# Optimization experiments

Hardware: AMD Instinct MI355X
Metric: run time of the kernel (lower is better)

## Reference

```python
import jax, jax.numpy as jnp
import numpy as np

K = 8               # config.k
X_MIN = -1.0        # x_min
X_MAX = 1.0         # x_max
GLOBAL_COEFF = 1.0  # config.global_coeff
EPS = 1e-8          # torch cosine_similarity eps
BZ, P, D = 8192, 1024, 1024  # batch, num_pool, data_dim


def setup_inputs() -> dict:
    key = jax.random.key(0)
    k1, k2, k3, k4, k5 = jax.random.split(key, 5)
    return {
        "ppg": jax.random.normal(k1, (BZ, 1, D), dtype=jnp.float32),
        "keys_pool": jax.random.normal(k2, (P, D), dtype=jnp.float32),
        "prompt_pool": jax.random.normal(k3, (P, D), dtype=jnp.float32),
        "cnn_w": jax.random.normal(k4, (1, 1, 3), dtype=jnp.float32) * 0.5,
        "cnn_b": jax.random.normal(k5, (1,), dtype=jnp.float32) * 0.1,
    }


def _prompt_cnn(prompt, w, b):
    # PromptCNN: Conv1d(1,1,k=3,pad=1) + ReLU on [P, D]
    x = prompt[:, None, :]  # [P, 1, D]
    y = jax.lax.conv_general_dilated(
        x, w, window_strides=(1,), padding=((1, 1),),
        dimension_numbers=("NCH", "OIH", "NCH"))
    y = jax.nn.relu(y + b[None, :, None])
    return y[:, 0, :]  # [P, D]


def _global_normalizer(prompt, x_min, x_max):
    pmax = jnp.max(prompt, axis=-1, keepdims=True)
    pmin = jnp.min(prompt, axis=-1, keepdims=True)
    scale = (x_max - x_min) / (pmax - pmin)
    return scale * (prompt - pmin) + x_min


def reference(ppg, keys_pool, prompt_pool, cnn_w, cnn_b):
    # prompt pool through CNN
    pcnn = _prompt_cnn(prompt_pool, cnn_w, cnn_b)  # [P, D]

    # cosine similarity: ppg [bz,1,D] vs keys [P,D] -> [bz,P]
    pn = ppg[:, 0, :] / jnp.maximum(
        jnp.linalg.norm(ppg[:, 0, :], axis=-1, keepdims=True), EPS)
    kn = keys_pool / jnp.maximum(
        jnp.linalg.norm(keys_pool, axis=-1, keepdims=True), EPS)
    cos = jnp.einsum("bd,pd->bp", pn, kn)  # [bz, P]
    score_ = 1.0 - cos

    # top-k smallest distances (largest=False) -> ascending order
    neg_vals, idx = jax.lax.top_k(-score_, K)  # [bz, K]
    score = -neg_vals

    # entropy of softmax over raw scores
    logp = jax.nn.log_softmax(score_, axis=-1)
    entropy = -(jnp.exp(logp) * logp).sum(axis=-1).mean()

    # gather selected prompts, average over k, add singleton channel dim
    prompt = pcnn[idx].mean(axis=1)[:, None, :]  # [bz, 1, D]

    # min-max global normalization (glonorm=True)
    prompt = _global_normalizer(prompt, X_MIN, X_MAX)

    # additive combine (mul=False)
    prompted = ppg + GLOBAL_COEFF * prompt  # [bz, 1, D]

    return prompted, score.mean(), entropy
```

## Files before the change

kernel.cpp:

```cpp
#include <hip/hip_runtime.h>
#include <hip/hip_bf16.h>

#define BZ 8192
#define PP 1024
#define DD 1024
#define KSEL 8

typedef unsigned short u16;
typedef __attribute__((ext_vector_type(8))) short bf16x8;
typedef __attribute__((ext_vector_type(4))) float f32x4;

#define WS_INVK 0
#define WS_INVP 1024
#define WS_SCORE 9216
#define WS_ENT 17408
#define WS_BF16_BYTE 368640ull

__device__ __forceinline__ u16 f2bf(float x) {
  __hip_bfloat16 h = __float2bfloat16(x);
  return *(u16*)&h;
}
__device__ __forceinline__ float bf2f(u16 u) {
  __hip_bfloat16 h; *(u16*)&h = u;
  return __bfloat162float(h);
}
__device__ __forceinline__ void gll16(const void* g, void* l) {
  __builtin_amdgcn_global_load_lds((__attribute__((address_space(1))) void*)g,
                                   (__attribute__((address_space(3))) void*)l, 16, 0, 0);
}

__global__ __launch_bounds__(256) void convert_kernel(const float* __restrict__ ppg,
                                                      const float* __restrict__ keys,
                                                      float* __restrict__ ws) {
  u16* Ahi = (u16*)((char*)ws + WS_BF16_BYTE);
  u16* Alo = Ahi + 8388608;
  u16* Bhi = Alo + 8388608;
  u16* Blo = Bhi + 1048576;

  int blk = blockIdx.x;
  const float* src; u16 *hi, *lo; float* invdst;
  if (blk < PP) {
    src = keys + (size_t)blk * DD;
    hi = Bhi + (size_t)blk * DD; lo = Blo + (size_t)blk * DD;
    invdst = ws + WS_INVK + blk;
  } else {
    int r = blk - PP;
    src = ppg + (size_t)r * DD;
    hi = Ahi + (size_t)r * DD; lo = Alo + (size_t)r * DD;
    invdst = ws + WS_INVP + r;
  }
  int t = threadIdx.x;
  float4 v = ((const float4*)src)[t];
  float x[4] = {v.x, v.y, v.z, v.w};
  u16 h4[4], l4[4];
  float s = 0.f;
  #pragma unroll
  for (int j = 0; j < 4; ++j) {
    h4[j] = f2bf(x[j]);
    l4[j] = f2bf(x[j] - bf2f(h4[j]));
    s += x[j] * x[j];
  }
  *(ushort4*)(hi + t * 4) = *(ushort4*)h4;
  *(ushort4*)(lo + t * 4) = *(ushort4*)l4;

  __shared__ float red[4];
  #pragma unroll
  for (int o = 32; o > 0; o >>= 1) s += __shfl_down(s, o);
  if ((t & 63) == 0) red[t >> 6] = s;
  __syncthreads();
  if (t == 0) {
    float tot = red[0] + red[1] + red[2] + red[3];
    *invdst = 1.0f / fmaxf(sqrtf(tot), 1e-8f);
  }
}

#define LDS_AH 0
#define LDS_AL 8192
#define LDS_BH 16384
#define LDS_BL 24576

__global__ __launch_bounds__(256, 2) void gemm_mfma(const float* __restrict__ ws_ro,
                                                    float* __restrict__ C) {
  const u16* Ahi = (const u16*)((const char*)ws_ro + WS_BF16_BYTE);
  const u16* Alo = Ahi + 8388608;
  const u16* Bhi = Alo + 8388608;
  const u16* Blo = Bhi + 1048576;

  __shared__ u16 lds[32768];

  int t = threadIdx.x;
  int wid = t >> 6, lane = t & 63;
  int lr = lane & 15, lg = lane >> 4;

  int orig = blockIdx.x;
  int wg = (orig & 7) * 64 + (orig >> 3);
  int bm0 = (wg >> 3) * 128;
  int bn0 = (wg & 7) * 128;
  int wm = wid >> 1, wn = wid & 1;

  size_t offA[4], offB[4];
  int ldso[4];
  #pragma unroll
  for (int r = 0; r < 4; ++r) {
    int s = r * 256 + t;
    int row = s >> 3, g = s & 7;
    offA[r] = (size_t)(bm0 + row) * DD + g * 8;
    offB[r] = (size_t)(bn0 + row) * DD + g * 8;
    ldso[r] = (r * 256 + wid * 64) * 8;
  }

  f32x4 acc[4][4] = {};

  for (int kt = 0; kt < 16; ++kt) {
    int k0 = kt * 64;
    #pragma unroll
    for (int r = 0; r < 4; ++r) {
      gll16(Ahi + offA[r] + k0, &lds[LDS_AH + ldso[r]]);
      gll16(Alo + offA[r] + k0, &lds[LDS_AL + ldso[r]]);
      gll16(Bhi + offB[r] + k0, &lds[LDS_BH + ldso[r]]);
      gll16(Blo + offB[r] + k0, &lds[LDS_BL + ldso[r]]);
    }
    __syncthreads();

    #pragma unroll
    for (int kh = 0; kh < 2; ++kh) {
      bf16x8 ah[4], al[4], bh[4], bl[4];
      #pragma unroll
      for (int i = 0; i < 4; ++i) {
        int off = (wm * 64 + i * 16 + lr) * 64 + kh * 32 + lg * 8;
        ah[i] = *(const bf16x8*)&lds[LDS_AH + off];
        al[i] = *(const bf16x8*)&lds[LDS_AL + off];
      }
      #pragma unroll
      for (int j = 0; j < 4; ++j) {
        int off = (wn * 64 + j * 16 + lr) * 64 + kh * 32 + lg * 8;
        bh[j] = *(const bf16x8*)&lds[LDS_BH + off];
        bl[j] = *(const bf16x8*)&lds[LDS_BL + off];
      }
      #pragma unroll
      for (int i = 0; i < 4; ++i)
        #pragma unroll
        for (int j = 0; j < 4; ++j) {
          acc[i][j] = __builtin_amdgcn_mfma_f32_16x16x32_bf16(ah[i], bh[j], acc[i][j], 0, 0, 0);
          acc[i][j] = __builtin_amdgcn_mfma_f32_16x16x32_bf16(ah[i], bl[j], acc[i][j], 0, 0, 0);
          acc[i][j] = __builtin_amdgcn_mfma_f32_16x16x32_bf16(al[i], bh[j], acc[i][j], 0, 0, 0);
        }
    }
    __syncthreads();
  }

  const float* invP = ws_ro + WS_INVP;
  const float* invK = ws_ro + WS_INVK;
  #pragma unroll
  for (int i = 0; i < 4; ++i) {
    #pragma unroll
    for (int q = 0; q < 4; ++q) {
      int row = bm0 + wm * 64 + i * 16 + lg * 4 + q;
      float ip = invP[row];
      #pragma unroll
      for (int j = 0; j < 4; ++j) {
        int col = bn0 + wn * 64 + j * 16 + lr;
        C[(size_t)row * PP + col] = acc[i][j][q] * ip * invK[col];
      }
    }
  }
}

__global__ __launch_bounds__(256) void fused_wave_topk_prompt(
    const float* __restrict__ ppg, const float* __restrict__ pool,
    const float* __restrict__ cw, const float* __restrict__ cb,
    float* __restrict__ ws, float* __restrict__ out) {
  int wid = threadIdx.x >> 6, lane = threadIdx.x & 63;
  int row = blockIdx.x * 4 + wid;
  const float* crow = out + (size_t)row * PP;

  float c[16];
  #pragma unroll
  for (int p = 0; p < 4; ++p) {
    f32x4 v = *(const f32x4*)(crow + p * 256 + lane * 4);
    c[p * 4 + 0] = v[0]; c[p * 4 + 1] = v[1]; c[p * 4 + 2] = v[2]; c[p * 4 + 3] = v[3];
  }

  {
    float z = 0.f, w = 0.f;
    #pragma unroll
    for (int l = 0; l < 16; ++l) {
      float s = 1.0f - c[l];
      float e = __expf(s - 2.0f);
      z += e; w += s * e;
    }
    #pragma unroll
    for (int o = 1; o < 64; o <<= 1) { z += __shfl_xor(z, o); w += __shfl_xor(w, o); }
    if (lane == 0) ws[WS_ENT + row] = 2.0f + __logf(z) - w / z;
  }

  unsigned used = 0;
  float score_sum = 0.f;
  int myidx = 0;
  #pragma unroll
  for (int it = 0; it < KSEL; ++it) {
    float v = -2.0f; int gi = 1 << 30;
    #pragma unroll
    for (int l = 0; l < 16; ++l) {
      if (!((used >> l) & 1u)) {
        float cv = c[l];
        int g = ((l >> 2) << 8) | (lane << 2) | (l & 3);
        if (cv > v || (cv == v && g < gi)) { v = cv; gi = g; }
      }
    }
    #pragma unroll
    for (int o = 1; o < 64; o <<= 1) {
      float ov = __shfl_xor(v, o);
      int og = __shfl_xor(gi, o);
      if (ov > v || (ov == v && og < gi)) { v = ov; gi = og; }
    }
    score_sum += 1.0f - v;
    if (((gi >> 2) & 63) == lane) used |= 1u << ((((gi >> 8) & 3) << 2) | (gi & 3));
    if (lane == it) myidx = gi;
  }
  if (lane == 0) ws[WS_SCORE + row] = score_sum;

  const float* prow = ppg + (size_t)row * DD;
  f32x4 pv[4];
  #pragma unroll
  for (int j = 0; j < 4; ++j)
    pv[j] = *(const f32x4*)(prow + j * 256 + lane * 4);

  float w0 = cw[0], w1 = cw[1], w2 = cw[2], bb = cb[0];
  float a[16] = {};
  #pragma unroll
  for (int s = 0; s < KSEL; ++s) {
    int rj = __shfl(myidx, s);
    const float* src = pool + (size_t)rj * DD;
    #pragma unroll
    for (int j = 0; j < 4; ++j) {
      int d0 = j * 256 + lane * 4;
      f32x4 x = *(const f32x4*)(src + d0);
      float xm = (d0 > 0) ? src[d0 - 1] : 0.f;
      float xp = (d0 + 4 < DD) ? src[d0 + 4] : 0.f;
      float y0 = fmaf(w0, xm,   fmaf(w1, x[0], fmaf(w2, x[1], bb)));
      float y1 = fmaf(w0, x[0], fmaf(w1, x[1], fmaf(w2, x[2], bb)));
      float y2 = fmaf(w0, x[1], fmaf(w1, x[2], fmaf(w2, x[3], bb)));
      float y3 = fmaf(w0, x[2], fmaf(w1, x[3], fmaf(w2, xp,   bb)));
      a[j * 4 + 0] += fmaxf(y0, 0.f);
      a[j * 4 + 1] += fmaxf(y1, 0.f);
      a[j * 4 + 2] += fmaxf(y2, 0.f);
      a[j * 4 + 3] += fmaxf(y3, 0.f);
    }
  }
  #pragma unroll
  for (int l = 0; l < 16; ++l) a[l] *= 0.125f;

  float lmin = a[0], lmax = a[0];
  #pragma unroll
  for (int l = 1; l < 16; ++l) { lmin = fminf(lmin, a[l]); lmax = fmaxf(lmax, a[l]); }
  #pragma unroll
  for (int o = 1; o < 64; o <<= 1) {
    lmin = fminf(lmin, __shfl_xor(lmin, o));
    lmax = fmaxf(lmax, __shfl_xor(lmax, o));
  }
  float scale = 2.0f / (lmax - lmin);

  float* orow = out + (size_t)row * DD;
  #pragma unroll
  for (int j = 0; j < 4; ++j) {
    f32x4 o4;
    #pragma unroll
    for (int q = 0; q < 4; ++q)
      o4[q] = pv[j][q] + (scale * (a[j * 4 + q] - lmin) - 1.0f);
    *(f32x4*)(orow + j * 256 + lane * 4) = o4;
  }
}

__global__ __launch_bounds__(256) void finalize_kernel(const float* __restrict__ ws,
                                                       float* __restrict__ out) {
  int t = threadIdx.x;
  const float* ss = ws + WS_SCORE;
  const float* ee = ws + WS_ENT;
  float s = 0.f, e = 0.f;
  for (int i = t; i < BZ; i += 256) { s += ss[i]; e += ee[i]; }
  __shared__ float rs[4], re[4];
  #pragma unroll
  for (int o = 32; o > 0; o >>= 1) { s += __shfl_down(s, o); e += __shfl_down(e, o); }
  if ((t & 63) == 0) { rs[t >> 6] = s; re[t >> 6] = e; }
  __syncthreads();
  if (t == 0) {
    float sT = rs[0] + rs[1] + rs[2] + rs[3];
    float eT = re[0] + re[1] + re[2] + re[3];
    out[(size_t)BZ * DD + 0] = sT / (float)(BZ * KSEL);
    out[(size_t)BZ * DD + 1] = eT / (float)BZ;
  }
}

extern "C" void kernel_launch(void* const* d_in, const int* in_sizes, int n_in,
                              void* d_out, int out_size, void* d_ws, size_t ws_size,
                              hipStream_t stream) {
  const float* ppg  = (const float*)d_in[0];
  const float* keys = (const float*)d_in[1];
  const float* pool = (const float*)d_in[2];
  const float* cw   = (const float*)d_in[3];
  const float* cb   = (const float*)d_in[4];
  float* out = (float*)d_out;
  float* ws  = (float*)d_ws;

  hipLaunchKernelGGL(convert_kernel, dim3(PP + BZ), dim3(256), 0, stream, ppg, keys, ws);
  hipLaunchKernelGGL(gemm_mfma, dim3((BZ / 128) * (PP / 128)), dim3(256), 0, stream, ws, out);
  hipLaunchKernelGGL(fused_wave_topk_prompt, dim3(BZ / 4), dim3(256), 0, stream,
                     ppg, pool, cw, cb, ws, out);
  hipLaunchKernelGGL(finalize_kernel, dim3(1), dim3(256), 0, stream, ws, out);
}
```

Measured before the change: 153.4 us.

## Split top-k and prompt gather into separate kernels with block-per-row prompt

```diff
diff --git a/kernel.cpp b/kernel.cpp
--- a/kernel.cpp
+++ b/kernel.cpp
@@ -14,6 +14,7 @@
 #define WS_INVP 1024
 #define WS_SCORE 9216
 #define WS_ENT 17408
+#define WS_IDX 25600
 #define WS_BF16_BYTE 368640ull
 
 __device__ __forceinline__ u16 f2bf(float x) {
@@ -166,13 +167,11 @@
   }
 }
 
-__global__ __launch_bounds__(256) void fused_wave_topk_prompt(
-    const float* __restrict__ ppg, const float* __restrict__ pool,
-    const float* __restrict__ cw, const float* __restrict__ cb,
-    float* __restrict__ ws, float* __restrict__ out) {
+__global__ __launch_bounds__(256) void topk_wave_kernel(const float* __restrict__ cosm,
+                                                        float* __restrict__ ws) {
   int wid = threadIdx.x >> 6, lane = threadIdx.x & 63;
   int row = blockIdx.x * 4 + wid;
-  const float* crow = out + (size_t)row * PP;
+  const float* crow = cosm + (size_t)row * PP;
 
   float c[16];
   #pragma unroll
@@ -181,18 +180,16 @@
     c[p * 4 + 0] = v[0]; c[p * 4 + 1] = v[1]; c[p * 4 + 2] = v[2]; c[p * 4 + 3] = v[3];
   }
 
-  {
-    float z = 0.f, w = 0.f;
-    #pragma unroll
-    for (int l = 0; l < 16; ++l) {
-      float s = 1.0f - c[l];
-      float e = __expf(s - 2.0f);
-      z += e; w += s * e;
-    }
-    #pragma unroll
-    for (int o = 1; o < 64; o <<= 1) { z += __shfl_xor(z, o); w += __shfl_xor(w, o); }
-    if (lane == 0) ws[WS_ENT + row] = 2.0f + __logf(z) - w / z;
-  }
+  float z = 0.f, w = 0.f;
+  #pragma unroll
+  for (int l = 0; l < 16; ++l) {
+    float s = 1.0f - c[l];
+    float e = __expf(s - 2.0f);
+    z += e; w += s * e;
+  }
+  #pragma unroll
+  for (int o = 1; o < 64; o <<= 1) { z += __shfl_xor(z, o); w += __shfl_xor(w, o); }
+  if (lane == 0) ws[WS_ENT + row] = 2.0f + __logf(z) - w / z;
 
   unsigned used = 0;
   float score_sum = 0.f;
@@ -219,57 +216,67 @@
     if (lane == it) myidx = gi;
   }
   if (lane == 0) ws[WS_SCORE + row] = score_sum;
-
-  const float* prow = ppg + (size_t)row * DD;
-  f32x4 pv[4];
-  #pragma unroll
-  for (int j = 0; j < 4; ++j)
-    pv[j] = *(const f32x4*)(prow + j * 256 + lane * 4);
-
+  if (lane < KSEL) ((int*)(ws + WS_IDX))[row * KSEL + lane] = myidx;
+}
+
+__global__ __launch_bounds__(256) void prompt_kernel(const float* __restrict__ ppg,
+                                                     const float* __restrict__ pool,
+                                                     const float* __restrict__ cw,
+                                                     const float* __restrict__ cb,
+                                                     const float* __restrict__ ws,
+                                                     float* __restrict__ out) {
+  int row = blockIdx.x;
+  int t = threadIdx.x;
+  int lane = t & 63;
+  const int* idx = (const int*)(ws + WS_IDX) + row * KSEL;
   float w0 = cw[0], w1 = cw[1], w2 = cw[2], bb = cb[0];
-  float a[16] = {};
-  #pragma unroll
-  for (int s = 0; s < KSEL; ++s) {
-    int rj = __shfl(myidx, s);
-    const float* src = pool + (size_t)rj * DD;
-    #pragma unroll
-    for (int j = 0; j < 4; ++j) {
-      int d0 = j * 256 + lane * 4;
-      f32x4 x = *(const f32x4*)(src + d0);
-      float xm = (d0 > 0) ? src[d0 - 1] : 0.f;
-      float xp = (d0 + 4 < DD) ? src[d0 + 4] : 0.f;
-      float y0 = fmaf(w0, xm,   fmaf(w1, x[0], fmaf(w2, x[1], bb)));
-      float y1 = fmaf(w0, x[0], fmaf(w1, x[1], fmaf(w2, x[2], bb)));
-      float y2 = fmaf(w0, x[1], fmaf(w1, x[2], fmaf(w2, x[3], bb)));
-      float y3 = fmaf(w0, x[2], fmaf(w1, x[3], fmaf(w2, xp,   bb)));
-      a[j * 4 + 0] += fmaxf(y0, 0.f);
-      a[j * 4 + 1] += fmaxf(y1, 0.f);
-      a[j * 4 + 2] += fmaxf(y2, 0.f);
-      a[j * 4 + 3] += fmaxf(y3, 0.f);
-    }
-  }
-  #pragma unroll
-  for (int l = 0; l < 16; ++l) a[l] *= 0.125f;
-
-  float lmin = a[0], lmax = a[0];
-  #pragma unroll
-  for (int l = 1; l < 16; ++l) { lmin = fminf(lmin, a[l]); lmax = fmaxf(lmax, a[l]); }
-  #pragma unroll
-  for (int o = 1; o < 64; o <<= 1) {
-    lmin = fminf(lmin, __shfl_xor(lmin, o));
-    lmax = fmaxf(lmax, __shfl_xor(lmax, o));
-  }
-  float scale = 2.0f / (lmax - lmin);
-
-  float* orow = out + (size_t)row * DD;
-  #pragma unroll
-  for (int j = 0; j < 4; ++j) {
-    f32x4 o4;
-    #pragma unroll
-    for (int q = 0; q < 4; ++q)
-      o4[q] = pv[j][q] + (scale * (a[j * 4 + q] - lmin) - 1.0f);
-    *(f32x4*)(orow + j * 256 + lane * 4) = o4;
-  }
+  int d0 = t * 4;
+
+  float a0 = 0.f, a1 = 0.f, a2 = 0.f, a3 = 0.f;
+  #pragma unroll
+  for (int j = 0; j < KSEL; ++j) {
+    int r = idx[j];
+    const float* src = pool + (size_t)r * DD;
+    f32x4 x = *(const f32x4*)(src + d0);
+    float xm_n = __shfl_up(x[3], 1);
+    float xp_n = __shfl_down(x[0], 1);
+    float xm, xp;
+    if (lane == 0)       xm = (t > 0)   ? src[d0 - 1] : 0.f;
+    else                 xm = xm_n;
+    if (lane == 63)      xp = (t < 255) ? src[d0 + 4] : 0.f;
+    else                 xp = xp_n;
+    float y0 = fmaf(w0, xm,   fmaf(w1, x[0], fmaf(w2, x[1], bb)));
+    float y1 = fmaf(w0, x[0], fmaf(w1, x[1], fmaf(w2, x[2], bb)));
+    float y2 = fmaf(w0, x[1], fmaf(w1, x[2], fmaf(w2, x[3], bb)));
+    float y3 = fmaf(w0, x[2], fmaf(w1, x[3], fmaf(w2, xp,   bb)));
+    a0 += fmaxf(y0, 0.f);
+    a1 += fmaxf(y1, 0.f);
+    a2 += fmaxf(y2, 0.f);
+    a3 += fmaxf(y3, 0.f);
+  }
+  a0 *= 0.125f; a1 *= 0.125f; a2 *= 0.125f; a3 *= 0.125f;
+
+  __shared__ float rmin[4], rmax[4];
+  float lmin = fminf(fminf(a0, a1), fminf(a2, a3));
+  float lmax = fmaxf(fmaxf(a0, a1), fmaxf(a2, a3));
+  #pragma unroll
+  for (int o = 32; o > 0; o >>= 1) {
+    lmin = fminf(lmin, __shfl_down(lmin, o));
+    lmax = fmaxf(lmax, __shfl_down(lmax, o));
+  }
+  if ((t & 63) == 0) { rmin[t >> 6] = lmin; rmax[t >> 6] = lmax; }
+  __syncthreads();
+  float pmin = fminf(fminf(rmin[0], rmin[1]), fminf(rmin[2], rmin[3]));
+  float pmax = fmaxf(fmaxf(rmax[0], rmax[1]), fmaxf(rmax[2], rmax[3]));
+  float scale = 2.0f / (pmax - pmin);
+
+  f32x4 pv = *(const f32x4*)(ppg + (size_t)row * DD + d0);
+  f32x4 o4;
+  o4[0] = pv[0] + (scale * (a0 - pmin) - 1.0f);
+  o4[1] = pv[1] + (scale * (a1 - pmin) - 1.0f);
+  o4[2] = pv[2] + (scale * (a2 - pmin) - 1.0f);
+  o4[3] = pv[3] + (scale * (a3 - pmin) - 1.0f);
+  *(f32x4*)(out + (size_t)row * DD + d0) = o4;
 }
 
 __global__ __launch_bounds__(256) void finalize_kernel(const float* __restrict__ ws,
@@ -305,7 +312,7 @@
 
   hipLaunchKernelGGL(convert_kernel, dim3(PP + BZ), dim3(256), 0, stream, ppg, keys, ws);
   hipLaunchKernelGGL(gemm_mfma, dim3((BZ / 128) * (PP / 128)), dim3(256), 0, stream, ws, out);
-  hipLaunchKernelGGL(fused_wave_topk_prompt, dim3(BZ / 4), dim3(256), 0, stream,
-                     ppg, pool, cw, cb, ws, out);
+  hipLaunchKernelGGL(topk_wave_kernel, dim3(BZ / 4), dim3(256), 0, stream, out, ws);
+  hipLaunchKernelGGL(prompt_kernel, dim3(BZ), dim3(256), 0, stream, ppg, pool, cw, cb, ws, out);
   hipLaunchKernelGGL(finalize_kernel, dim3(1), dim3(256), 0, stream, ws, out);
 }
```

Measured after the change: 135.6 us. -11.6%, faster.
